# Performance work log

Hardware: AMD Instinct MI355X
Metric: run time of the kernel (lower is better)

Reference implementation:

```python
import jax, jax.numpy as jnp
import numpy as np

ALPHA = 10.0
BETA = 0.05
FAR_DELTA = 1e10  # matches torch 10000000000.0 padding for the last delta


def sdf_to_density(signed_distance, alpha, beta):
    s = -signed_distance
    return jnp.where(
        s <= 0,
        alpha * (0.5 * jnp.exp(s / beta)),
        alpha * (1.0 - 0.5 * jnp.exp(-s / beta)),
    )


def setup_inputs() -> dict:
    key = jax.random.key(0)
    k1, k2, k3 = jax.random.split(key, 3)
    R, N = 65536, 128
    distance = jax.random.normal(k1, (R, N), dtype=jnp.float32)  # SDF values
    color = jax.random.uniform(k2, (R, N, 3), dtype=jnp.float32)
    # per-ray sorted sample depths in [2, 6] (near/far)
    t = jax.random.uniform(k3, (R, N), dtype=jnp.float32)
    depth_values = jnp.sort(2.0 + 4.0 * t, axis=-1)
    return {"distance": distance, "color": color, "depth_values": depth_values}


def reference(distance, color, depth_values):
    # deltas: [R, N], last delta padded with a huge value
    deltas = jnp.concatenate(
        [depth_values[:, 1:] - depth_values[:, :-1],
         jnp.full_like(depth_values[:, :1], FAR_DELTA)],
        axis=-1,
    )
    density = sdf_to_density(distance, ALPHA, BETA)  # [R, N]
    d = density * deltas  # [R, N]
    # transmittance: exp(-cumsum of previous densities), exclusive scan
    trans = jnp.exp(-jnp.concatenate(
        [jnp.zeros_like(d[:, :1]), jnp.cumsum(d[:, :-1], axis=-1)], axis=-1))
    weights = (1.0 - jnp.exp(-d)) * trans  # [R, N]
    out_color = jnp.sum(weights[..., None] * color, axis=-2)  # [R, 3]
    geometry = jnp.zeros_like(color)  # faithful to geometry_color = zeros_like(color)
    return out_color, geometry
```

## Files before the change

kernel.cpp:

```cpp
#include <hip/hip_runtime.h>

#define ALPHA     10.0f
#define INV_BETA  20.0f
#define FAR_DELTA 1e10f
#define NSAMP     128
#define TCUT      8.0f

__device__ __forceinline__ float laplace_density(float sdf) {
    float s = -sdf;
    float e = __expf(-fabsf(s) * INV_BETA);
    return (s <= 0.f) ? (0.5f * ALPHA * e) : (ALPHA * (1.f - 0.5f * e));
}

__global__ __launch_bounds__(256) void volsdf_render(
    const float* __restrict__ dist,
    const float* __restrict__ color,
    const float* __restrict__ depth,
    float*       __restrict__ out,
    int R)
{
    const int lane   = threadIdx.x & 63;
    const int waveId = threadIdx.x >> 6;
    const int sub    = lane & 31;
    const int half   = lane >> 5;
    const int rayPair = blockIdx.x * 4 + waveId;
    const int ray     = rayPair * 2 + half;
    if (ray >= R) return;

    const size_t rbase = (size_t)ray * NSAMP;

    float4 di = ((const float4*)(dist  + rbase))[sub];
    float4 dp = ((const float4*)(depth + rbase))[sub];

    float nx  = __shfl_down(dp.x, 1, 32);
    float dl0 = dp.y - dp.x;
    float dl1 = dp.z - dp.y;
    float dl2 = dp.w - dp.z;
    float dl3 = (sub == 31) ? FAR_DELTA : (nx - dp.w);

    float d0 = laplace_density(di.x) * dl0;
    float d1 = laplace_density(di.y) * dl1;
    float d2 = laplace_density(di.z) * dl2;
    float d3 = laplace_density(di.w) * dl3;

    float local = (d0 + d1) + (d2 + d3);
    float incl  = local;
    #pragma unroll
    for (int off = 1; off < 32; off <<= 1) {
        float v = __shfl_up(incl, off, 32);
        if (sub >= off) incl += v;
    }
    float base = __shfl_up(incl, 1, 32);
    if (sub == 0) base = 0.f;

    float ar = 0.f, ag = 0.f, ab = 0.f;
    if (base < TCUT) {
        const float* cp = color + rbase * 3 + (size_t)sub * 12;
        float4 c0 = ((const float4*)cp)[0];
        float4 c1 = ((const float4*)cp)[1];
        float4 c2 = ((const float4*)cp)[2];

        float p1 = base + d0, p2 = p1 + d1, p3 = p2 + d2;
        float w0 = (1.f - __expf(-d0)) * __expf(-base);
        float w1 = (1.f - __expf(-d1)) * __expf(-p1);
        float w2 = (1.f - __expf(-d2)) * __expf(-p2);
        float w3 = (1.f - __expf(-d3)) * __expf(-p3);

        ar = (w0 * c0.x + w1 * c0.w) + (w2 * c1.z + w3 * c2.y);
        ag = (w0 * c0.y + w1 * c1.x) + (w2 * c1.w + w3 * c2.z);
        ab = (w0 * c0.z + w1 * c1.y) + (w2 * c2.x + w3 * c2.w);
    }

    #pragma unroll
    for (int off = 16; off > 0; off >>= 1) {
        ar += __shfl_down(ar, off, 32);
        ag += __shfl_down(ag, off, 32);
        ab += __shfl_down(ab, off, 32);
    }
    if (sub == 0) {
        out[(size_t)ray * 3 + 0] = ar;
        out[(size_t)ray * 3 + 1] = ag;
        out[(size_t)ray * 3 + 2] = ab;
    }
}

extern "C" void kernel_launch(void* const* d_in, const int* in_sizes, int n_in,
                              void* d_out, int out_size, void* d_ws, size_t ws_size,
                              hipStream_t stream) {
    const float* dist  = (const float*)d_in[0];
    const float* color = (const float*)d_in[1];
    const float* depth = (const float*)d_in[2];
    float* out = (float*)d_out;

    const int R = in_sizes[0] / NSAMP;
    const int blocks = (R + 7) / 8;

    hipMemsetAsync(d_out, 0, (size_t)out_size * sizeof(float), stream);

    hipLaunchKernelGGL(volsdf_render, dim3(blocks), dim3(256), 0, stream,
                       dist, color, depth, out, R);
}
```

Measured before the change: 213.7 us.

## Split ray into two halves and skip second-half loads when transmittance saturates

```diff
diff --git a/kernel.cpp b/kernel.cpp
--- a/kernel.cpp
+++ b/kernel.cpp
@@ -29,21 +29,14 @@
 
     const size_t rbase = (size_t)ray * NSAMP;
 
-    float4 di = ((const float4*)(dist  + rbase))[sub];
-    float4 dp = ((const float4*)(depth + rbase))[sub];
+    float2 di = ((const float2*)(dist  + rbase))[sub];
+    float2 dp = ((const float2*)(depth + rbase))[sub];
 
     float nx  = __shfl_down(dp.x, 1, 32);
-    float dl0 = dp.y - dp.x;
-    float dl1 = dp.z - dp.y;
-    float dl2 = dp.w - dp.z;
-    float dl3 = (sub == 31) ? FAR_DELTA : (nx - dp.w);
+    float da  = laplace_density(di.x) * (dp.y - dp.x);
+    float db  = (sub == 31) ? 0.f : laplace_density(di.y) * (nx - dp.y);
 
-    float d0 = laplace_density(di.x) * dl0;
-    float d1 = laplace_density(di.y) * dl1;
-    float d2 = laplace_density(di.z) * dl2;
-    float d3 = laplace_density(di.w) * dl3;
-
-    float local = (d0 + d1) + (d2 + d3);
+    float local = da + db;
     float incl  = local;
     #pragma unroll
     for (int off = 1; off < 32; off <<= 1) {
@@ -52,23 +45,61 @@
     }
     float base = __shfl_up(incl, 1, 32);
     if (sub == 0) base = 0.f;
+    float total_lo = __shfl(incl, 31, 32);
 
     float ar = 0.f, ag = 0.f, ab = 0.f;
-    if (base < TCUT) {
-        const float* cp = color + rbase * 3 + (size_t)sub * 12;
-        float4 c0 = ((const float4*)cp)[0];
-        float4 c1 = ((const float4*)cp)[1];
-        float4 c2 = ((const float4*)cp)[2];
+    float2 c01, c23, c45;
+    bool haveC = base < TCUT;
+    if (haveC) {
+        const float* cp = color + rbase * 3 + (size_t)sub * 6;
+        c01 = ((const float2*)cp)[0];
+        c23 = ((const float2*)cp)[1];
+        c45 = ((const float2*)cp)[2];
+        float wa = (1.f - __expf(-da)) * __expf(-base);
+        float wb = (1.f - __expf(-db)) * __expf(-(base + da));
+        ar = wa * c01.x + wb * c23.y;
+        ag = wa * c01.y + wb * c45.x;
+        ab = wa * c23.x + wb * c45.y;
+    }
 
-        float p1 = base + d0, p2 = p1 + d1, p3 = p2 + d2;
-        float w0 = (1.f - __expf(-d0)) * __expf(-base);
-        float w1 = (1.f - __expf(-d1)) * __expf(-p1);
-        float w2 = (1.f - __expf(-d2)) * __expf(-p2);
-        float w3 = (1.f - __expf(-d3)) * __expf(-p3);
+    if (total_lo < TCUT) {
+        float2 dt = ((const float2*)(dist  + rbase + 64))[sub];
+        float2 pt = ((const float2*)(depth + rbase + 64))[sub];
 
-        ar = (w0 * c0.x + w1 * c0.w) + (w2 * c1.z + w3 * c2.y);
-        ag = (w0 * c0.y + w1 * c1.x) + (w2 * c1.w + w3 * c2.z);
-        ab = (w0 * c0.z + w1 * c1.y) + (w2 * c2.x + w3 * c2.w);
+        float depth64 = __shfl(pt.x, 0, 32);
+        float d63l = laplace_density(di.y) * (depth64 - dp.y);
+        float d63  = __shfl(d63l, 31, 32);
+        if (sub == 31 && haveC) {
+            float w63 = (1.f - __expf(-d63)) * __expf(-(base + da));
+            ar += w63 * c23.y; ag += w63 * c45.x; ab += w63 * c45.y;
+        }
+
+        float nxt = __shfl_down(pt.x, 1, 32);
+        float ea  = laplace_density(dt.x) * (pt.y - pt.x);
+        float eb  = laplace_density(dt.y) *
+                    ((sub == 31) ? FAR_DELTA : (nxt - pt.y));
+        float loc2 = ea + eb;
+        float inc2 = loc2;
+        #pragma unroll
+        for (int off = 1; off < 32; off <<= 1) {
+            float v = __shfl_up(inc2, off, 32);
+            if (sub >= off) inc2 += v;
+        }
+        float base2 = __shfl_up(inc2, 1, 32);
+        if (sub == 0) base2 = 0.f;
+        base2 += total_lo + d63;
+
+        if (base2 < TCUT) {
+            const float* cp = color + (rbase + 64) * 3 + (size_t)sub * 6;
+            float2 t01 = ((const float2*)cp)[0];
+            float2 t23 = ((const float2*)cp)[1];
+            float2 t45 = ((const float2*)cp)[2];
+            float wa = (1.f - __expf(-ea)) * __expf(-base2);
+            float wb = (1.f - __expf(-eb)) * __expf(-(base2 + ea));
+            ar += wa * t01.x + wb * t23.y;
+            ag += wa * t01.y + wb * t45.x;
+            ab += wa * t23.x + wb * t45.y;
+        }
     }
 
     #pragma unroll
```

Result: faster. 207.9 us (-2.7%).
